# Kernel tuning notes

Hardware: AMD Instinct MI355X
Metric: run time of the kernel (lower is better)

Reference implementation:

```python
import jax, jax.numpy as jnp
import numpy as np

B, H, W, C = 1, 64, 64, 768
HEADS = 12
HD = C // HEADS  # 64


def setup_inputs() -> dict:
    key = jax.random.key(0)
    ks = jax.random.split(key, 11)
    s = 0.02
    return {
        "hidden_states": jax.random.normal(ks[0], (B, H, W, C), jnp.float32),
        "w_q": jax.random.normal(ks[1], (C, C), jnp.float32) * s,
        "b_q": jnp.zeros((C,), jnp.float32),
        "w_k": jax.random.normal(ks[2], (C, C), jnp.float32) * s,
        "b_k": jnp.zeros((C,), jnp.float32),
        "w_v": jax.random.normal(ks[3], (C, C), jnp.float32) * s,
        "b_v": jnp.zeros((C,), jnp.float32),
        "w_o": jax.random.normal(ks[4], (C, C), jnp.float32) * s,
        "b_o": jnp.zeros((C,), jnp.float32),
        "rel_pos_h": jax.random.normal(ks[5], (2 * H - 1, HD), jnp.float32) * s,
        "rel_pos_w": jax.random.normal(ks[6], (2 * W - 1, HD), jnp.float32) * s,
    }


def _get_rel_pos(q_size, k_size, rel_pos):
    # q_size == k_size here, so no interpolation branch; pure gather.
    coords = jnp.arange(q_size)[:, None] - jnp.arange(k_size)[None, :] + (k_size - 1)
    return rel_pos[coords]  # (q_size, k_size, head_dim)


def reference(hidden_states, w_q, b_q, w_k, b_k, w_v, b_v, w_o, b_o, rel_pos_h, rel_pos_w):
    b, h, w, c = hidden_states.shape
    hd = c // HEADS

    def proj(wm, bm):
        y = hidden_states @ wm.T + bm  # (b,h,w,c)
        return y.reshape(b, h * w, HEADS, hd).transpose(0, 2, 1, 3)  # (b,heads,hw,hd)

    q = proj(w_q, b_q)
    k = proj(w_k, b_k)
    v = proj(w_v, b_v)

    # decomposed relative position bias (per head-dim query)
    Rh = _get_rel_pos(h, h, rel_pos_h)  # (h,h,hd)
    Rw = _get_rel_pos(w, w, rel_pos_w)  # (w,w,hd)
    qr = q.reshape(b, HEADS, h, w, hd)
    rel_h = jnp.einsum('bnhwc,hkc->bnhwk', qr, Rh)  # (b,heads,h,w,h)
    rel_w = jnp.einsum('bnhwc,wkc->bnhwk', qr, Rw)  # (b,heads,h,w,w)
    attn_bias = (rel_h[..., :, None] + rel_w[..., None, :]).reshape(b, HEADS, h * w, h * w)

    scale = hd ** -0.5
    scores = jnp.einsum('bnqd,bnkd->bnqk', q, k) * scale + attn_bias
    attn = jax.nn.softmax(scores, axis=-1)
    out = jnp.einsum('bnqk,bnkd->bnqd', attn, v)  # (b,heads,hw,hd)
    out = out.transpose(0, 2, 1, 3).reshape(b, h, w, c)
    return out @ w_o.T + b_o
```

## Files before the change

kernel.cpp:

```cpp
#include <hip/hip_runtime.h>


typedef __attribute__((ext_vector_type(8))) short bf16x8;
typedef __attribute__((ext_vector_type(4))) float f32x4;
typedef __attribute__((ext_vector_type(4))) short s16x4;
typedef __attribute__((ext_vector_type(2))) unsigned int u32x2;

__device__ __forceinline__ float b2f(unsigned short h) {
    union { unsigned int u; float f; } v; v.u = ((unsigned int)h) << 16; return v.f;
}
__device__ __forceinline__ unsigned short f2b(float f) {
    union { float f; unsigned int u; } v; v.f = f;
    unsigned int r = v.u + 0x7FFFu + ((v.u >> 16) & 1u);
    return (unsigned short)(r >> 16);
}
__device__ __forceinline__ void gl_lds16(const void* g, void* l) {
    __builtin_amdgcn_global_load_lds(
        (const __attribute__((address_space(1))) void*)g,
        (__attribute__((address_space(3))) void*)l, 16, 0, 0);
}

__global__ __launch_bounds__(256) void cvt_bf16(
        const float* __restrict__ hs, const float* __restrict__ wq,
        const float* __restrict__ wk, const float* __restrict__ wv,
        const float* __restrict__ wo, const float* __restrict__ rph,
        const float* __restrict__ rpw, unsigned short* __restrict__ dst) {
    const int idx = blockIdx.x * 256 + threadIdx.x;
    if (idx >= 1380320) return;
    const float* src;
    int off;
    if      (idx < 786432)  { src = hs;  off = idx; }
    else if (idx < 933888)  { src = wq;  off = idx - 786432; }
    else if (idx < 1081344) { src = wk;  off = idx - 933888; }
    else if (idx < 1228800) { src = wv;  off = idx - 1081344; }
    else if (idx < 1376256) { src = wo;  off = idx - 1228800; }
    else if (idx < 1378288) { src = rph; off = idx - 1376256; }
    else                    { src = rpw; off = idx - 1378288; }
    const float4 v = ((const float4*)src)[off];
    s16x4 o;
    o[0] = (short)f2b(v.x); o[1] = (short)f2b(v.y);
    o[2] = (short)f2b(v.z); o[3] = (short)f2b(v.w);
    *(s16x4*)(dst + (size_t)idx * 4) = o;
}

__launch_bounds__(256, 3)
__global__ void qkv128(const unsigned short* __restrict__ X,
                       const unsigned short* __restrict__ Wq,
                       const unsigned short* __restrict__ Wk,
                       const unsigned short* __restrict__ Wv,
                       const float* __restrict__ bq,
                       const float* __restrict__ bk,
                       const float* __restrict__ bv,
                       unsigned short* __restrict__ qb,
                       unsigned short* __restrict__ kb,
                       unsigned short* __restrict__ vtb) {
    __shared__ __align__(16) unsigned short sarena[8192];
    unsigned short* abuf = sarena;
    unsigned short* bbuf = sarena + 4096;
    const int tid = threadIdx.x, lane = tid & 63, w = tid >> 6;
    const int r = lane & 15, quad = lane >> 4;
    const int nt = blockIdx.x, mt = blockIdx.y, z = blockIdx.z;
    const unsigned short* W  = (z == 0) ? Wq : (z == 1) ? Wk : Wv;
    const float*          Bv = (z == 0) ? bq : (z == 1) ? bk : bv;
    unsigned short*     outp = (z == 0) ? qb : (z == 1) ? kb : vtb;

    const int c0 = w * 64 + lane, c1 = c0 + 256;
    const unsigned short* xs0 = X + (mt * 128 + (c0 & 127)) * 768 + (c0 >> 7) * 8;
    const unsigned short* xs1 = X + (mt * 128 + (c1 & 127)) * 768 + (c1 >> 7) * 8;
    const unsigned short* ws0 = W + (nt * 128 + (c0 & 127)) * 768 + (c0 >> 7) * 8;
    const unsigned short* ws1 = W + (nt * 128 + (c1 & 127)) * 768 + (c1 >> 7) * 8;

    const int wr = (w & 1) * 64, wc = (w >> 1) * 64;
    f32x4 acc[4][4] = {};
    for (int kt = 0; kt < 24; ++kt) {
        gl_lds16(xs0 + kt * 32, &abuf[w * 512]);
        gl_lds16(xs1 + kt * 32, &abuf[2048 + w * 512]);
        gl_lds16(ws0 + kt * 32, &bbuf[w * 512]);
        gl_lds16(ws1 + kt * 32, &bbuf[2048 + w * 512]);
        __syncthreads();
        bf16x8 af[4], bfr[4];
#pragma unroll
        for (int i = 0; i < 4; ++i)
            af[i] = *(const bf16x8*)&abuf[(quad * 128 + wr + i * 16 + r) * 8];
#pragma unroll
        for (int j = 0; j < 4; ++j)
            bfr[j] = *(const bf16x8*)&bbuf[(quad * 128 + wc + j * 16 + r) * 8];
#pragma unroll
        for (int i = 0; i < 4; ++i)
#pragma unroll
            for (int j = 0; j < 4; ++j)
                acc[i][j] = __builtin_amdgcn_mfma_f32_16x16x32_bf16(af[i], bfr[j], acc[i][j], 0, 0, 0);
        __syncthreads();
    }
    if (z < 2) {
#pragma unroll
        for (int j = 0; j < 4; ++j) {
            const int n = nt * 128 + wc + j * 16 + r;
            const float bias = Bv[n];
            const int nhi = n >> 6, nlo = n & 63;
#pragma unroll
            for (int i = 0; i < 4; ++i) {
#pragma unroll
                for (int reg = 0; reg < 4; ++reg) {
                    const int m = mt * 128 + wr + i * 16 + quad * 4 + reg;
                    outp[(nhi * 4096 + m) * 64 + nlo] = f2b(acc[i][j][reg] + bias);
                }
            }
        }
    } else {
#pragma unroll
        for (int pass = 0; pass < 2; ++pass) {
            if ((w >> 1) == pass) {
#pragma unroll
                for (int j = 0; j < 4; ++j) {
                    const int n_l = j * 16 + r;
                    const float bias = Bv[nt * 128 + pass * 64 + n_l];
                    const int sw = (n_l & 7) << 4;
#pragma unroll
                    for (int reg = 0; reg < 4; ++reg) {
                        const int tokb = (wr + (quad * 4 + reg) * 4) ^ sw;
                        u32x2 d2;
                        d2.x = (unsigned int)f2b(acc[0][j][reg] + bias)
                             | ((unsigned int)f2b(acc[1][j][reg] + bias) << 16);
                        d2.y = (unsigned int)f2b(acc[2][j][reg] + bias)
                             | ((unsigned int)f2b(acc[3][j][reg] + bias) << 16);
                        *(u32x2*)&sarena[n_l * 128 + tokb] = d2;
                    }
                }
            }
            __syncthreads();
#pragma unroll
            for (int c = 0; c < 4; ++c) {
                const int u = c * 256 + tid;
                const int n_l = u >> 4, g = u & 15;
                const int phys = n_l * 128 + ((g * 8) ^ ((n_l & 7) << 4));
                bf16x8 val = *(const bf16x8*)&sarena[phys];
                *(bf16x8*)&outp[(size_t)(nt * 128 + pass * 64 + n_l) * 4096
                                + mt * 128 + g * 8] = val;
            }
            __syncthreads();
        }
    }
}

__launch_bounds__(256, 3)
__global__ void out128(const unsigned short* __restrict__ X,
                       const unsigned short* __restrict__ W,
                       const float* __restrict__ Bv,
                       float* __restrict__ out) {
    __shared__ __align__(16) unsigned short abuf[4 * 128 * 8];
    __shared__ __align__(16) unsigned short bbuf[4 * 128 * 8];
    const int tid = threadIdx.x, lane = tid & 63, w = tid >> 6;
    const int r = lane & 15, quad = lane >> 4;
    const int nt = blockIdx.x, mt = blockIdx.y;

    const int c0 = w * 64 + lane, c1 = c0 + 256;
    const unsigned short* xs0 = X + (mt * 128 + (c0 & 127)) * 768 + (c0 >> 7) * 8;
    const unsigned short* xs1 = X + (mt * 128 + (c1 & 127)) * 768 + (c1 >> 7) * 8;
    const unsigned short* ws0 = W + (nt * 128 + (c0 & 127)) * 768 + (c0 >> 7) * 8;
    const unsigned short* ws1 = W + (nt * 128 + (c1 & 127)) * 768 + (c1 >> 7) * 8;

    const int wr = (w & 1) * 64, wc = (w >> 1) * 64;
    f32x4 acc[4][4] = {};
    for (int kt = 0; kt < 24; ++kt) {
        gl_lds16(xs0 + kt * 32, &abuf[w * 512]);
        gl_lds16(xs1 + kt * 32, &abuf[2048 + w * 512]);
        gl_lds16(ws0 + kt * 32, &bbuf[w * 512]);
        gl_lds16(ws1 + kt * 32, &bbuf[2048 + w * 512]);
        __syncthreads();
        bf16x8 af[4], bfr[4];
#pragma unroll
        for (int i = 0; i < 4; ++i)
            af[i] = *(const bf16x8*)&abuf[(quad * 128 + wr + i * 16 + r) * 8];
#pragma unroll
        for (int j = 0; j < 4; ++j)
            bfr[j] = *(const bf16x8*)&bbuf[(quad * 128 + wc + j * 16 + r) * 8];
#pragma unroll
        for (int i = 0; i < 4; ++i)
#pragma unroll
            for (int j = 0; j < 4; ++j)
                acc[i][j] = __builtin_amdgcn_mfma_f32_16x16x32_bf16(af[i], bfr[j], acc[i][j], 0, 0, 0);
        __syncthreads();
    }
#pragma unroll
    for (int j = 0; j < 4; ++j) {
        const int n = nt * 128 + wc + j * 16 + r;
        const float bias = Bv[n];
#pragma unroll
        for (int i = 0; i < 4; ++i) {
#pragma unroll
            for (int reg = 0; reg < 4; ++reg) {
                const int m = mt * 128 + wr + i * 16 + quad * 4 + reg;
                out[m * 768 + n] = acc[i][j][reg] + bias;
            }
        }
    }
}

__launch_bounds__(256, 4)
__global__ void relk(const unsigned short* __restrict__ qbuf,
                     const unsigned short* __restrict__ rph,
                     const unsigned short* __restrict__ rpw,
                     unsigned short* __restrict__ rh,
                     unsigned short* __restrict__ rw) {
    __shared__ __align__(16) unsigned short abuf[8 * 64 * 8];
    __shared__ __align__(16) unsigned short bbuf[8 * 64 * 8];
    const int tid = threadIdx.x;
    const int lane = tid & 63, w = tid >> 6;
    const int r = lane & 15, quad = lane >> 4;
    const int a = blockIdx.x, h = blockIdx.y, mode = blockIdx.z;
    const unsigned short* rp = mode ? rpw : rph;
    const float osc = mode ? 1.0f : 1.44269504f;

#pragma unroll
    for (int gg = 0; gg < 2; ++gg) {
        const int g = w * 2 + gg;
        const int arow = mode ? (h * 4096 + lane * 64 + a) : (h * 4096 + a * 64 + lane);
        gl_lds16(qbuf + arow * 64 + g * 8, &abuf[g * 512]);
        const int bidx = a - lane + 63;
        gl_lds16(rp + bidx * 64 + g * 8, &bbuf[g * 512]);
    }
    __syncthreads();

    f32x4 acc[4] = {};
#pragma unroll
    for (int s = 0; s < 2; ++s) {
        bf16x8 af = *(const bf16x8*)&abuf[((s * 4 + quad) * 64 + w * 16 + r) * 8];
#pragma unroll
        for (int j = 0; j < 4; ++j) {
            bf16x8 bfr = *(const bf16x8*)&bbuf[((s * 4 + quad) * 64 + j * 16 + r) * 8];
            acc[j] = __builtin_amdgcn_mfma_f32_16x16x32_bf16(af, bfr, acc[j], 0, 0, 0);
        }
    }
    unsigned short* out = mode ? rw : rh;
#pragma unroll
    for (int j = 0; j < 4; ++j) {
#pragma unroll
        for (int reg = 0; reg < 4; ++reg) {
            const int m = w * 16 + quad * 4 + reg, n = j * 16 + r;
            const int t = mode ? (h * 4096 + m * 64 + a) : (h * 4096 + a * 64 + m);
            out[t * 64 + n] = f2b(acc[j][reg] * osc);
        }
    }
}

__launch_bounds__(256, 3)
__global__ void attn2(const unsigned short* __restrict__ qbuf,
                      const unsigned short* __restrict__ kbuf,
                      const unsigned short* __restrict__ vtbuf,
                      const unsigned short* __restrict__ rhb,
                      const unsigned short* __restrict__ rwb,
                      float* __restrict__ po, float* __restrict__ lp) {
    __shared__ __align__(16) unsigned short skb[4096];
    __shared__ __align__(16) unsigned short svb[4096];
    __shared__ __align__(16) unsigned short spb[9216];
    __shared__ __align__(16) unsigned short srh[8192];
    const int tid = threadIdx.x;
    const int lane = tid & 63, w = tid >> 6;
    const int r = lane & 15, quad = lane >> 4;
    const int qt = blockIdx.x, h = blockIdx.y, sp = blockIdx.z;
    const float L2E = 1.44269504f;
    const float SC = 0.125f * L2E;

#pragma unroll
    for (int i = 0; i < 4; ++i) {
        const int gp = i * 2 + (w >> 1), ql = (w & 1) * 64 + lane;
        gl_lds16(rhb + (h * 4096 + qt * 128 + ql) * 64 + gp * 8,
                 &srh[(i * 256 + w * 64) * 8]);
    }
    bf16x8 qf[2][2];
#pragma unroll
    for (int g = 0; g < 2; ++g) {
        const unsigned short* qrow =
            qbuf + (h * 4096 + qt * 128 + g * 64 + w * 16 + r) * 64;
        qf[g][0] = *(const bf16x8*)(qrow + quad * 8);
        qf[g][1] = *(const bf16x8*)(qrow + 32 + quad * 8);
    }
    float rwL[2][4][4];
#pragma unroll
    for (int g = 0; g < 2; ++g) {
        const unsigned short* rwrow = rwb + (h * 4096 + qt * 128 + g * 64) * 64;
#pragma unroll
        for (int reg = 0; reg < 4; ++reg) {
            const int ql = w * 16 + quad * 4 + reg;
#pragma unroll
            for (int j = 0; j < 4; ++j)
                rwL[g][j][reg] = b2f(rwrow[ql * 64 + j * 16 + r]) * L2E;
        }
    }
    bf16x8 onesf;
#pragma unroll
    for (int i = 0; i < 8; ++i) onesf[i] = (short)0x3F80;

    f32x4 lacc[2] = {};
    f32x4 oacc[2][4] = {};
    __syncthreads();

    for (int tl = 0; tl < 32; ++tl) {
        const int t = sp * 32 + tl;
#pragma unroll
        for (int gg = 0; gg < 2; ++gg) {
            const int g = w * 2 + gg;
            gl_lds16(kbuf + (h * 4096 + t * 64 + lane) * 64 + g * 8, &skb[g * 512]);
            gl_lds16(vtbuf + (h * 64 + lane) * 4096 + t * 64 + g * 8, &svb[g * 512]);
        }
        __syncthreads();

        f32x4 s0[4] = {}, s1[4] = {};
#pragma unroll
        for (int s2 = 0; s2 < 2; ++s2) {
#pragma unroll
            for (int j = 0; j < 4; ++j) {
                bf16x8 kf = *(const bf16x8*)&skb[((s2 * 4 + quad) * 64 + j * 16 + r) * 8];
                s0[j] = __builtin_amdgcn_mfma_f32_16x16x32_bf16(qf[0][s2], kf, s0[j], 0, 0, 0);
                s1[j] = __builtin_amdgcn_mfma_f32_16x16x32_bf16(qf[1][s2], kf, s1[j], 0, 0, 0);
            }
        }
#pragma unroll
        for (int g = 0; g < 2; ++g) {
            float rh2[4];
#pragma unroll
            for (int reg = 0; reg < 4; ++reg)
                rh2[reg] = b2f(srh[((t >> 3) * 128 + g * 64 + w * 16 + quad * 4 + reg) * 8
                                   + (t & 7)]);
#pragma unroll
            for (int reg = 0; reg < 4; ++reg) {
                unsigned int u[4];
#pragma unroll
                for (int j = 0; j < 4; ++j) {
                    const float sv = g ? s1[j][reg] : s0[j][reg];
                    const float p = __builtin_amdgcn_exp2f(
                        fmaf(sv, SC, rh2[reg] + rwL[g][j][reg]));
                    union { float f; unsigned int q; } cv; cv.f = p;
                    u[j] = cv.q;
                }
                u32x2 d;
                d.x = __builtin_amdgcn_perm(u[1], u[0], 0x07060302);
                d.y = __builtin_amdgcn_perm(u[3], u[2], 0x07060302);
                *(u32x2*)&spb[g * 4608 + w * 1152 + (quad * 4 + reg) * 72 + r * 4] = d;
            }
        }
#pragma unroll
        for (int s = 0; s < 2; ++s) {
            bf16x8 pf0 = *(const bf16x8*)&spb[w * 1152 + r * 72 + s * 32 + quad * 8];
            bf16x8 pf1 = *(const bf16x8*)&spb[4608 + w * 1152 + r * 72 + s * 32 + quad * 8];
            lacc[0] = __builtin_amdgcn_mfma_f32_16x16x32_bf16(pf0, onesf, lacc[0], 0, 0, 0);
            lacc[1] = __builtin_amdgcn_mfma_f32_16x16x32_bf16(pf1, onesf, lacc[1], 0, 0, 0);
#pragma unroll
            for (int j = 0; j < 4; ++j) {
                bf16x8 vf = *(const bf16x8*)&svb[((s * 4 + quad) * 64 + j * 16 + r) * 8];
                oacc[0][j] = __builtin_amdgcn_mfma_f32_16x16x32_bf16(pf0, vf, oacc[0][j], 0, 0, 0);
                oacc[1][j] = __builtin_amdgcn_mfma_f32_16x16x32_bf16(pf1, vf, oacc[1][j], 0, 0, 0);
            }
        }
        __syncthreads();
    }
    const size_t pbase = ((size_t)(sp * 12 + h) * 4096 + qt * 128);
#pragma unroll
    for (int g = 0; g < 2; ++g) {
        const int qrow = g * 64 + w * 16 + quad * 4;
#pragma unroll
        for (int reg = 0; reg < 4; ++reg) {
#pragma unroll
            for (int j = 0; j < 4; ++j)
                po[(pbase + qrow + reg) * 64 + j * 16 + r] = oacc[g][j][reg];
            if (r == 0) lp[pbase + qrow + reg] = lacc[g][reg];
        }
    }
}

__global__ __launch_bounds__(256) void combine(const float* __restrict__ po,
                                               const float* __restrict__ lp,
                                               unsigned short* __restrict__ ab) {
    const unsigned int idx = blockIdx.x * 256 + threadIdx.x;
    const unsigned int tok = idx / 96u;
    const unsigned int part = idx - tok * 96u;
    const int c = part * 8, h = c >> 6, d = c & 63;
    const float* p0 = po + ((size_t)h * 4096 + tok) * 64 + d;
    const float* p1 = po + ((size_t)(12 + h) * 4096 + tok) * 64 + d;
    const float inv = 1.f / (lp[h * 4096 + tok] + lp[(12 + h) * 4096 + tok]);
    const float4 a0 = *(const float4*)p0, b0 = *(const float4*)(p0 + 4);
    const float4 a1 = *(const float4*)p1, b1 = *(const float4*)(p1 + 4);
    s16x4 o0, o1;
    o0[0] = (short)f2b((a0.x + a1.x) * inv); o0[1] = (short)f2b((a0.y + a1.y) * inv);
    o0[2] = (short)f2b((a0.z + a1.z) * inv); o0[3] = (short)f2b((a0.w + a1.w) * inv);
    o1[0] = (short)f2b((b0.x + b1.x) * inv); o1[1] = (short)f2b((b0.y + b1.y) * inv);
    o1[2] = (short)f2b((b0.z + b1.z) * inv); o1[3] = (short)f2b((b0.w + b1.w) * inv);
    unsigned short* dst = ab + (size_t)tok * 768 + c;
    *(s16x4*)dst = o0;
    *(s16x4*)(dst + 4) = o1;
}

extern "C" void kernel_launch(void* const* d_in, const int* in_sizes, int n_in,
                              void* d_out, int out_size, void* d_ws, size_t ws_size,
                              hipStream_t stream) {
    const float* hs  = (const float*)d_in[0];
    const float* wq  = (const float*)d_in[1];
    const float* bq  = (const float*)d_in[2];
    const float* wk  = (const float*)d_in[3];
    const float* bk  = (const float*)d_in[4];
    const float* wv  = (const float*)d_in[5];
    const float* bv  = (const float*)d_in[6];
    const float* wo  = (const float*)d_in[7];
    const float* bo  = (const float*)d_in[8];
    const float* rph = (const float*)d_in[9];
    const float* rpw = (const float*)d_in[10];

    unsigned short* ws = (unsigned short*)d_ws;
    const int HS = 3145728, WN = 589824, RP = 8128;
    const int HB = 12 * 4096 * 64;
    unsigned short* hsb  = ws;
    unsigned short* wqb  = hsb  + HS;
    unsigned short* wkb  = wqb  + WN;
    unsigned short* wvb  = wkb  + WN;
    unsigned short* wob  = wvb  + WN;
    unsigned short* rphb = wob  + WN;
    unsigned short* rpwb = rphb + RP;
    unsigned short* qb   = rpwb + RP;
    unsigned short* kb   = qb   + HB;
    unsigned short* vtb  = kb   + HB;
    unsigned short* rhb  = vtb  + HB;
    unsigned short* rwb  = rhb  + HB;
    unsigned short* ab   = rwb  + HB;
    float* po = (float*)(ab + HB);
    float* lp = po + 2 * 12 * 4096 * 64;

    cvt_bf16<<<dim3((1380320 + 255) / 256), 256, 0, stream>>>(
        hs, wq, wk, wv, wo, rph, rpw, hsb);
    qkv128<<<dim3(6, 32, 3), 256, 0, stream>>>(
        hsb, wqb, wkb, wvb, bq, bk, bv, qb, kb, vtb);
    relk<<<dim3(64, 12, 2), 256, 0, stream>>>(qb, rphb, rpwb, rhb, rwb);
    attn2<<<dim3(32, 12, 2), 256, 0, stream>>>(qb, kb, vtb, rhb, rwb, po, lp);
    combine<<<dim3(1536), 256, 0, stream>>>(po, lp, ab);
    out128<<<dim3(6, 32), 256, 0, stream>>>(ab, wob, bo, (float*)d_out);
}
```

Before: 247.6 us.

## Prefetch next K/V tile into registers and add MFMA priority hints in attention

Replaces the per-iteration direct global-to-LDS loads of K and V^T with register prefetch of the next tile, issued before the current tile's compute and written to LDS after it. The goal is to hide global memory latency behind the QK and PV MFMA work. It also adds s_setprio around the MFMA blocks and loads only the rel_h slice this split needs, halving that shared buffer. The cost is extra VGPRs for the prefetch registers, which may hurt occupancy under the 3-blocks launch bound, plus a second barrier per iteration.

```diff
diff --git a/kernel.cpp b/kernel.cpp
--- a/kernel.cpp
+++ b/kernel.cpp
@@ -5,6 +5,7 @@
 typedef __attribute__((ext_vector_type(4))) float f32x4;
 typedef __attribute__((ext_vector_type(4))) short s16x4;
 typedef __attribute__((ext_vector_type(2))) unsigned int u32x2;
+typedef __attribute__((ext_vector_type(4))) unsigned int u32x4;
 
 __device__ __forceinline__ float b2f(unsigned short h) {
     union { unsigned int u; float f; } v; v.u = ((unsigned int)h) << 16; return v.f;
@@ -254,7 +255,7 @@
     __shared__ __align__(16) unsigned short skb[4096];
     __shared__ __align__(16) unsigned short svb[4096];
     __shared__ __align__(16) unsigned short spb[9216];
-    __shared__ __align__(16) unsigned short srh[8192];
+    __shared__ __align__(16) unsigned short srh[4096];
     const int tid = threadIdx.x;
     const int lane = tid & 63, w = tid >> 6;
     const int r = lane & 15, quad = lane >> 4;
@@ -263,9 +264,9 @@
     const float SC = 0.125f * L2E;
 
 #pragma unroll
-    for (int i = 0; i < 4; ++i) {
-        const int gp = i * 2 + (w >> 1), ql = (w & 1) * 64 + lane;
-        gl_lds16(rhb + (h * 4096 + qt * 128 + ql) * 64 + gp * 8,
+    for (int i = 0; i < 2; ++i) {
+        const int ql = (w & 1) * 64 + lane;
+        gl_lds16(rhb + (h * 4096 + qt * 128 + ql) * 64 + (sp * 4 + i * 2 + (w >> 1)) * 8,
                  &srh[(i * 256 + w * 64) * 8]);
     }
     bf16x8 qf[2][2];
@@ -292,21 +293,37 @@
 #pragma unroll
     for (int i = 0; i < 8; ++i) onesf[i] = (short)0x3F80;
 
+    const unsigned short* ksrc = kbuf + (size_t)(h * 4096 + lane) * 64 + w * 16;
+    const unsigned short* vsrc = vtbuf + (size_t)(h * 64 + lane) * 4096 + w * 16;
+    u32x4 kp0, kp1, vp0, vp1;
+    {
+        const int t0 = sp * 32;
+        kp0 = *(const u32x4*)(ksrc + (size_t)t0 * 4096);
+        kp1 = *(const u32x4*)(ksrc + (size_t)t0 * 4096 + 8);
+        vp0 = *(const u32x4*)(vsrc + t0 * 64);
+        vp1 = *(const u32x4*)(vsrc + t0 * 64 + 8);
+    }
+
     f32x4 lacc[2] = {};
     f32x4 oacc[2][4] = {};
     __syncthreads();
+    *(u32x4*)&skb[(w * 128 + lane) * 8]      = kp0;
+    *(u32x4*)&skb[(w * 128 + 64 + lane) * 8] = kp1;
+    *(u32x4*)&svb[(w * 128 + lane) * 8]      = vp0;
+    *(u32x4*)&svb[(w * 128 + 64 + lane) * 8] = vp1;
+    __syncthreads();
 
     for (int tl = 0; tl < 32; ++tl) {
         const int t = sp * 32 + tl;
-#pragma unroll
-        for (int gg = 0; gg < 2; ++gg) {
-            const int g = w * 2 + gg;
-            gl_lds16(kbuf + (h * 4096 + t * 64 + lane) * 64 + g * 8, &skb[g * 512]);
-            gl_lds16(vtbuf + (h * 64 + lane) * 4096 + t * 64 + g * 8, &svb[g * 512]);
-        }
-        __syncthreads();
+        if (tl < 31) {
+            kp0 = *(const u32x4*)(ksrc + (size_t)(t + 1) * 4096);
+            kp1 = *(const u32x4*)(ksrc + (size_t)(t + 1) * 4096 + 8);
+            vp0 = *(const u32x4*)(vsrc + (t + 1) * 64);
+            vp1 = *(const u32x4*)(vsrc + (t + 1) * 64 + 8);
+        }
 
         f32x4 s0[4] = {}, s1[4] = {};
+        __builtin_amdgcn_s_setprio(1);
 #pragma unroll
         for (int s2 = 0; s2 < 2; ++s2) {
 #pragma unroll
@@ -316,12 +333,13 @@
                 s1[j] = __builtin_amdgcn_mfma_f32_16x16x32_bf16(qf[1][s2], kf, s1[j], 0, 0, 0);
             }
         }
+        __builtin_amdgcn_s_setprio(0);
 #pragma unroll
         for (int g = 0; g < 2; ++g) {
             float rh2[4];
 #pragma unroll
             for (int reg = 0; reg < 4; ++reg)
-                rh2[reg] = b2f(srh[((t >> 3) * 128 + g * 64 + w * 16 + quad * 4 + reg) * 8
+                rh2[reg] = b2f(srh[((tl >> 3) * 128 + g * 64 + w * 16 + quad * 4 + reg) * 8
                                    + (t & 7)]);
 #pragma unroll
             for (int reg = 0; reg < 4; ++reg) {
@@ -340,6 +358,7 @@
                 *(u32x2*)&spb[g * 4608 + w * 1152 + (quad * 4 + reg) * 72 + r * 4] = d;
             }
         }
+        __builtin_amdgcn_s_setprio(1);
 #pragma unroll
         for (int s = 0; s < 2; ++s) {
             bf16x8 pf0 = *(const bf16x8*)&spb[w * 1152 + r * 72 + s * 32 + quad * 8];
@@ -352,6 +371,15 @@
                 oacc[0][j] = __builtin_amdgcn_mfma_f32_16x16x32_bf16(pf0, vf, oacc[0][j], 0, 0, 0);
                 oacc[1][j] = __builtin_amdgcn_mfma_f32_16x16x32_bf16(pf1, vf, oacc[1][j], 0, 0, 0);
             }
+        }
+        __builtin_amdgcn_s_setprio(0);
+
+        __syncthreads();
+        if (tl < 31) {
+            *(u32x4*)&skb[(w * 128 + lane) * 8]      = kp0;
+            *(u32x4*)&skb[(w * 128 + 64 + lane) * 8] = kp1;
+            *(u32x4*)&svb[(w * 128 + lane) * 8]      = vp0;
+            *(u32x4*)&svb[(w * 128 + 64 + lane) * 8] = vp1;
         }
         __syncthreads();
     }
```

After: 232.8 us. -6.0%, faster.

## Double-buffer GEMM and attention tiles, fold softmax scales into Q and bias

Applied to the files above, without the earlier changes.

Adds double-buffered LDS staging to the QKV and output projection GEMMs and to the attention K/V tiles, so the next tile's global-to-LDS loads are issued before the current tile's MFMAs. Folds the attention scale and log2(e) into Q at projection time and into the rel-pos bias precompute, and seeds the score accumulators with the bias so the exp2 needs no fma. Replaces the LDS staging of rel_h with per-lane register prefetch and adds s_setprio around the MFMA blocks. LDS per block doubles for the GEMMs, which may reduce occupancy. The scale folding changes bf16 rounding points.

```diff
diff --git a/kernel.cpp b/kernel.cpp
--- a/kernel.cpp
+++ b/kernel.cpp
@@ -54,15 +54,14 @@
                        unsigned short* __restrict__ qb,
                        unsigned short* __restrict__ kb,
                        unsigned short* __restrict__ vtb) {
-    __shared__ __align__(16) unsigned short sarena[8192];
-    unsigned short* abuf = sarena;
-    unsigned short* bbuf = sarena + 4096;
+    __shared__ __align__(16) unsigned short sarena[16384];
     const int tid = threadIdx.x, lane = tid & 63, w = tid >> 6;
     const int r = lane & 15, quad = lane >> 4;
     const int nt = blockIdx.x, mt = blockIdx.y, z = blockIdx.z;
     const unsigned short* W  = (z == 0) ? Wq : (z == 1) ? Wk : Wv;
     const float*          Bv = (z == 0) ? bq : (z == 1) ? bk : bv;
     unsigned short*     outp = (z == 0) ? qb : (z == 1) ? kb : vtb;
+    const float qsc = (z == 0) ? 0.18033688f : 1.0f;
 
     const int c0 = w * 64 + lane, c1 = c0 + 256;
     const unsigned short* xs0 = X + (mt * 128 + (c0 & 127)) * 768 + (c0 >> 7) * 8;
@@ -70,27 +69,40 @@
     const unsigned short* ws0 = W + (nt * 128 + (c0 & 127)) * 768 + (c0 >> 7) * 8;
     const unsigned short* ws1 = W + (nt * 128 + (c1 & 127)) * 768 + (c1 >> 7) * 8;
 
+    gl_lds16(xs0, &sarena[w * 512]);
+    gl_lds16(xs1, &sarena[2048 + w * 512]);
+    gl_lds16(ws0, &sarena[4096 + w * 512]);
+    gl_lds16(ws1, &sarena[4096 + 2048 + w * 512]);
+    __syncthreads();
+
     const int wr = (w & 1) * 64, wc = (w >> 1) * 64;
     f32x4 acc[4][4] = {};
+    int cur = 0;
+#pragma unroll 2
     for (int kt = 0; kt < 24; ++kt) {
-        gl_lds16(xs0 + kt * 32, &abuf[w * 512]);
-        gl_lds16(xs1 + kt * 32, &abuf[2048 + w * 512]);
-        gl_lds16(ws0 + kt * 32, &bbuf[w * 512]);
-        gl_lds16(ws1 + kt * 32, &bbuf[2048 + w * 512]);
-        __syncthreads();
+        if (kt < 23) {
+            const int nx = (cur ^ 1) * 8192;
+            gl_lds16(xs0 + (kt + 1) * 32, &sarena[nx + w * 512]);
+            gl_lds16(xs1 + (kt + 1) * 32, &sarena[nx + 2048 + w * 512]);
+            gl_lds16(ws0 + (kt + 1) * 32, &sarena[nx + 4096 + w * 512]);
+            gl_lds16(ws1 + (kt + 1) * 32, &sarena[nx + 4096 + 2048 + w * 512]);
+        }
+        const unsigned short* ab = &sarena[cur * 8192];
+        const unsigned short* bb = ab + 4096;
         bf16x8 af[4], bfr[4];
 #pragma unroll
         for (int i = 0; i < 4; ++i)
-            af[i] = *(const bf16x8*)&abuf[(quad * 128 + wr + i * 16 + r) * 8];
+            af[i] = *(const bf16x8*)&ab[(quad * 128 + wr + i * 16 + r) * 8];
 #pragma unroll
         for (int j = 0; j < 4; ++j)
-            bfr[j] = *(const bf16x8*)&bbuf[(quad * 128 + wc + j * 16 + r) * 8];
+            bfr[j] = *(const bf16x8*)&bb[(quad * 128 + wc + j * 16 + r) * 8];
 #pragma unroll
         for (int i = 0; i < 4; ++i)
 #pragma unroll
             for (int j = 0; j < 4; ++j)
                 acc[i][j] = __builtin_amdgcn_mfma_f32_16x16x32_bf16(af[i], bfr[j], acc[i][j], 0, 0, 0);
         __syncthreads();
+        cur ^= 1;
     }
     if (z < 2) {
 #pragma unroll
@@ -103,7 +115,7 @@
 #pragma unroll
                 for (int reg = 0; reg < 4; ++reg) {
                     const int m = mt * 128 + wr + i * 16 + quad * 4 + reg;
-                    outp[(nhi * 4096 + m) * 64 + nlo] = f2b(acc[i][j][reg] + bias);
+                    outp[(nhi * 4096 + m) * 64 + nlo] = f2b((acc[i][j][reg] + bias) * qsc);
                 }
             }
         }
@@ -148,8 +160,7 @@
                        const unsigned short* __restrict__ W,
                        const float* __restrict__ Bv,
                        float* __restrict__ out) {
-    __shared__ __align__(16) unsigned short abuf[4 * 128 * 8];
-    __shared__ __align__(16) unsigned short bbuf[4 * 128 * 8];
+    __shared__ __align__(16) unsigned short sarena[16384];
     const int tid = threadIdx.x, lane = tid & 63, w = tid >> 6;
     const int r = lane & 15, quad = lane >> 4;
     const int nt = blockIdx.x, mt = blockIdx.y;
@@ -160,27 +171,40 @@
     const unsigned short* ws0 = W + (nt * 128 + (c0 & 127)) * 768 + (c0 >> 7) * 8;
     const unsigned short* ws1 = W + (nt * 128 + (c1 & 127)) * 768 + (c1 >> 7) * 8;
 
+    gl_lds16(xs0, &sarena[w * 512]);
+    gl_lds16(xs1, &sarena[2048 + w * 512]);
+    gl_lds16(ws0, &sarena[4096 + w * 512]);
+    gl_lds16(ws1, &sarena[4096 + 2048 + w * 512]);
+    __syncthreads();
+
     const int wr = (w & 1) * 64, wc = (w >> 1) * 64;
     f32x4 acc[4][4] = {};
+    int cur = 0;
+#pragma unroll 2
     for (int kt = 0; kt < 24; ++kt) {
-        gl_lds16(xs0 + kt * 32, &abuf[w * 512]);
-        gl_lds16(xs1 + kt * 32, &abuf[2048 + w * 512]);
-        gl_lds16(ws0 + kt * 32, &bbuf[w * 512]);
-        gl_lds16(ws1 + kt * 32, &bbuf[2048 + w * 512]);
-        __syncthreads();
+        if (kt < 23) {
+            const int nx = (cur ^ 1) * 8192;
+            gl_lds16(xs0 + (kt + 1) * 32, &sarena[nx + w * 512]);
+            gl_lds16(xs1 + (kt + 1) * 32, &sarena[nx + 2048 + w * 512]);
+            gl_lds16(ws0 + (kt + 1) * 32, &sarena[nx + 4096 + w * 512]);
+            gl_lds16(ws1 + (kt + 1) * 32, &sarena[nx + 4096 + 2048 + w * 512]);
+        }
+        const unsigned short* ab = &sarena[cur * 8192];
+        const unsigned short* bb = ab + 4096;
         bf16x8 af[4], bfr[4];
 #pragma unroll
         for (int i = 0; i < 4; ++i)
-            af[i] = *(const bf16x8*)&abuf[(quad * 128 + wr + i * 16 + r) * 8];
+            af[i] = *(const bf16x8*)&ab[(quad * 128 + wr + i * 16 + r) * 8];
 #pragma unroll
         for (int j = 0; j < 4; ++j)
-            bfr[j] = *(const bf16x8*)&bbuf[(quad * 128 + wc + j * 16 + r) * 8];
+            bfr[j] = *(const bf16x8*)&bb[(quad * 128 + wc + j * 16 + r) * 8];
 #pragma unroll
         for (int i = 0; i < 4; ++i)
 #pragma unroll
             for (int j = 0; j < 4; ++j)
                 acc[i][j] = __builtin_amdgcn_mfma_f32_16x16x32_bf16(af[i], bfr[j], acc[i][j], 0, 0, 0);
         __syncthreads();
+        cur ^= 1;
     }
 #pragma unroll
     for (int j = 0; j < 4; ++j) {
@@ -210,7 +234,7 @@
     const int r = lane & 15, quad = lane >> 4;
     const int a = blockIdx.x, h = blockIdx.y, mode = blockIdx.z;
     const unsigned short* rp = mode ? rpw : rph;
-    const float osc = mode ? 1.0f : 1.44269504f;
+    const float osc = 8.0f;
 
 #pragma unroll
     for (int gg = 0; gg < 2; ++gg) {
@@ -251,23 +275,30 @@
                       const unsigned short* __restrict__ rhb,
                       const unsigned short* __restrict__ rwb,
                       float* __restrict__ po, float* __restrict__ lp) {
-    __shared__ __align__(16) unsigned short skb[4096];
-    __shared__ __align__(16) unsigned short svb[4096];
+    __shared__ __align__(16) unsigned short skb[2][4096];
+    __shared__ __align__(16) unsigned short svb[2][4096];
     __shared__ __align__(16) unsigned short spb[9216];
-    __shared__ __align__(16) unsigned short srh[8192];
     const int tid = threadIdx.x;
     const int lane = tid & 63, w = tid >> 6;
     const int r = lane & 15, quad = lane >> 4;
     const int qt = blockIdx.x, h = blockIdx.y, sp = blockIdx.z;
-    const float L2E = 1.44269504f;
-    const float SC = 0.125f * L2E;
-
-#pragma unroll
-    for (int i = 0; i < 4; ++i) {
-        const int gp = i * 2 + (w >> 1), ql = (w & 1) * 64 + lane;
-        gl_lds16(rhb + (h * 4096 + qt * 128 + ql) * 64 + gp * 8,
-                 &srh[(i * 256 + w * 64) * 8]);
-    }
+
+    {
+        const int t0 = sp * 32;
+#pragma unroll
+        for (int gg = 0; gg < 2; ++gg) {
+            const int g = w * 2 + gg;
+            gl_lds16(kbuf + (h * 4096 + t0 * 64 + lane) * 64 + g * 8, &skb[0][g * 512]);
+            gl_lds16(vtbuf + (h * 64 + lane) * 4096 + t0 * 64 + g * 8, &svb[0][g * 512]);
+        }
+    }
+    const unsigned short* rhp =
+        rhb + (size_t)(h * 4096 + qt * 128 + w * 16 + quad * 4) * 64;
+    unsigned short rhu[8];
+#pragma unroll
+    for (int i = 0; i < 8; ++i)
+        rhu[i] = rhp[((i >> 2) * 64 + (i & 3)) * 64 + sp * 32];
+
     bf16x8 qf[2][2];
 #pragma unroll
     for (int g = 0; g < 2; ++g) {
@@ -285,7 +316,7 @@
             const int ql = w * 16 + quad * 4 + reg;
 #pragma unroll
             for (int j = 0; j < 4; ++j)
-                rwL[g][j][reg] = b2f(rwrow[ql * 64 + j * 16 + r]) * L2E;
+                rwL[g][j][reg] = b2f(rwrow[ql * 64 + j * 16 + r]);
         }
     }
     bf16x8 onesf;
@@ -296,41 +327,55 @@
     f32x4 oacc[2][4] = {};
     __syncthreads();
 
+    int cur = 0;
+#pragma unroll 2
     for (int tl = 0; tl < 32; ++tl) {
         const int t = sp * 32 + tl;
-#pragma unroll
-        for (int gg = 0; gg < 2; ++gg) {
-            const int g = w * 2 + gg;
-            gl_lds16(kbuf + (h * 4096 + t * 64 + lane) * 64 + g * 8, &skb[g * 512]);
-            gl_lds16(vtbuf + (h * 64 + lane) * 4096 + t * 64 + g * 8, &svb[g * 512]);
-        }
-        __syncthreads();
-
-        f32x4 s0[4] = {}, s1[4] = {};
+        if (tl < 31) {
+#pragma unroll
+            for (int gg = 0; gg < 2; ++gg) {
+                const int g = w * 2 + gg;
+                gl_lds16(kbuf + (h * 4096 + (t + 1) * 64 + lane) * 64 + g * 8,
+                         &skb[cur ^ 1][g * 512]);
+                gl_lds16(vtbuf + (h * 64 + lane) * 4096 + (t + 1) * 64 + g * 8,
+                         &svb[cur ^ 1][g * 512]);
+            }
+        }
+        float rh2f[8];
+#pragma unroll
+        for (int i = 0; i < 8; ++i) rh2f[i] = b2f(rhu[i]);
+        if (tl < 31) {
+#pragma unroll
+            for (int i = 0; i < 8; ++i)
+                rhu[i] = rhp[((i >> 2) * 64 + (i & 3)) * 64 + (t + 1)];
+        }
+        f32x4 s0[4], s1[4];
+#pragma unroll
+        for (int j = 0; j < 4; ++j)
+#pragma unroll
+            for (int reg = 0; reg < 4; ++reg) {
+                s0[j][reg] = rh2f[reg]     + rwL[0][j][reg];
+                s1[j][reg] = rh2f[4 + reg] + rwL[1][j][reg];
+            }
+        __builtin_amdgcn_s_setprio(1);
 #pragma unroll
         for (int s2 = 0; s2 < 2; ++s2) {
 #pragma unroll
             for (int j = 0; j < 4; ++j) {
-                bf16x8 kf = *(const bf16x8*)&skb[((s2 * 4 + quad) * 64 + j * 16 + r) * 8];
+                bf16x8 kf = *(const bf16x8*)&skb[cur][((s2 * 4 + quad) * 64 + j * 16 + r) * 8];
                 s0[j] = __builtin_amdgcn_mfma_f32_16x16x32_bf16(qf[0][s2], kf, s0[j], 0, 0, 0);
                 s1[j] = __builtin_amdgcn_mfma_f32_16x16x32_bf16(qf[1][s2], kf, s1[j], 0, 0, 0);
             }
         }
+        __builtin_amdgcn_s_setprio(0);
 #pragma unroll
         for (int g = 0; g < 2; ++g) {
-            float rh2[4];
-#pragma unroll
-            for (int reg = 0; reg < 4; ++reg)
-                rh2[reg] = b2f(srh[((t >> 3) * 128 + g * 64 + w * 16 + quad * 4 + reg) * 8
-                                   + (t & 7)]);
 #pragma unroll
             for (int reg = 0; reg < 4; ++reg) {
                 unsigned int u[4];
 #pragma unroll
                 for (int j = 0; j < 4; ++j) {
-                    const float sv = g ? s1[j][reg] : s0[j][reg];
-                    const float p = __builtin_amdgcn_exp2f(
-                        fmaf(sv, SC, rh2[reg] + rwL[g][j][reg]));
+                    const float p = __builtin_amdgcn_exp2f(g ? s1[j][reg] : s0[j][reg]);
                     union { float f; unsigned int q; } cv; cv.f = p;
                     u[j] = cv.q;
                 }
@@ -340,6 +385,7 @@
                 *(u32x2*)&spb[g * 4608 + w * 1152 + (quad * 4 + reg) * 72 + r * 4] = d;
             }
         }
+        __builtin_amdgcn_s_setprio(1);
 #pragma unroll
         for (int s = 0; s < 2; ++s) {
             bf16x8 pf0 = *(const bf16x8*)&spb[w * 1152 + r * 72 + s * 32 + quad * 8];
@@ -348,12 +394,15 @@
             lacc[1] = __builtin_amdgcn_mfma_f32_16x16x32_bf16(pf1, onesf, lacc[1], 0, 0, 0);
 #pragma unroll
             for (int j = 0; j < 4; ++j) {
-                bf16x8 vf = *(const bf16x8*)&svb[((s * 4 + quad) * 64 + j * 16 + r) * 8];
+                bf16x8 vf = *(const bf16x8*)&svb[cur][((s * 4 + quad) * 64 + j * 16 + r) * 8];
                 oacc[0][j] = __builtin_amdgcn_mfma_f32_16x16x32_bf16(pf0, vf, oacc[0][j], 0, 0, 0);
                 oacc[1][j] = __builtin_amdgcn_mfma_f32_16x16x32_bf16(pf1, vf, oacc[1][j], 0, 0, 0);
             }
         }
+        __builtin_amdgcn_s_setprio(0);
+
         __syncthreads();
+        cur ^= 1;
     }
     const size_t pbase = ((size_t)(sp * 12 + h) * 4096 + qt * 128);
 #pragma unroll
```

After: 241.0 us. 1.03x faster.
